# Kernel tuning notes

Measured on AMD Instinct MI355X. Metric: run time of the kernel, lower is better.

Reference implementation:

```python
import jax, jax.numpy as jnp
import numpy as np

B, N, IN, H, L, C = 2048, 100, 64, 256, 3, 3
NEG_SLOPE = 0.2


def setup_inputs() -> dict:
    key = jax.random.key(0)
    ks = jax.random.split(key, 11)
    s = lambda k, sh: jax.random.normal(k, sh, dtype=jnp.float32) * 0.05
    return {
        'x': jax.random.normal(ks[0], (B, N, IN), dtype=jnp.float32),
        'W_exp': s(ks[1], (IN, H)), 'b_exp': s(ks[2], (H,)),
        'W_l': s(ks[3], (L, H, H)), 'b_l': s(ks[4], (L, H)),
        'W_r': s(ks[5], (L, H, H)), 'b_r': s(ks[6], (L, H)),
        'att': s(ks[7], (L, H)), 'bias': s(ks[8], (L, H)),
        'W_fc': s(ks[9], (H, C)), 'b_fc': s(ks[10], (C,)),
    }


def _make_pe(n, d):
    pos = jnp.arange(n, dtype=jnp.float32)[:, None]
    div = jnp.exp(jnp.arange(0, d, 2, dtype=jnp.float32) * (-jnp.log(jnp.float32(10000.0)) / d))
    pe = jnp.zeros((n, d), dtype=jnp.float32)
    pe = pe.at[:, 0::2].set(jnp.sin(pos * div))
    pe = pe.at[:, 1::2].set(jnp.cos(pos * div))
    return pe


def _edges(n):
    # bidirectional chain + self loops (GATv2Conv add_self_loops=True)
    src = np.concatenate([np.arange(n - 1), np.arange(1, n), np.arange(n)])
    dst = np.concatenate([np.arange(1, n), np.arange(n - 1), np.arange(n)])
    return jnp.asarray(src), jnp.asarray(dst)


def _gatv2_conv(x, src, dst, Wl, bl, Wr, br, a, b, n):
    # x: [B,N,H]; PyG GATv2Conv, heads=1, share_weights=False
    xl = x @ Wl + bl                      # source transform [B,N,H]
    xr = x @ Wr + br                      # target transform [B,N,H]
    m = jax.nn.leaky_relu(xl[:, src] + xr[:, dst], NEG_SLOPE)   # [B,E,H]
    logits = jnp.einsum('beh,h->be', m, a)                      # [B,E]
    seg_max = jax.vmap(lambda l: jax.ops.segment_max(l, dst, num_segments=n))(logits)
    ex = jnp.exp(logits - seg_max[:, dst])
    denom = jax.vmap(lambda e: jax.ops.segment_sum(e, dst, num_segments=n))(ex)
    alpha = ex / denom[:, dst]                                  # [B,E]
    msgs = alpha[:, :, None] * xl[:, src]                       # [B,E,H]
    out = jax.vmap(lambda mm: jax.ops.segment_sum(mm, dst, num_segments=n))(msgs)
    return out + b


def reference(x, W_exp, b_exp, W_l, b_l, W_r, b_r, att, bias, W_fc, b_fc):
    n = x.shape[1]
    src, dst = _edges(n)
    x0 = x @ W_exp + b_exp + _make_pe(n, W_exp.shape[1])   # expander + positional encoding
    # Faithful to original: the loop feeds batch.x (= x0) into every conv layer,
    # so the output of the loop is the LAST conv applied to x0.
    h = x0
    for l in range(W_l.shape[0]):
        h = _gatv2_conv(x0, src, dst, W_l[l], b_l[l], W_r[l], b_r[l], att[l], bias[l], n)
    pooled = h.sum(axis=1)                                 # global_add_pool -> [B,H]
    return pooled @ W_fc + b_fc                            # [B,num_classes]
```

## Files before the change

### kernel.cpp

```cpp
#include <hip/hip_runtime.h>
#include <hip/hip_bf16.h>
#include <hip/hip_fp16.h>

#define BB 2048
#define NN 100
#define INF_ 64
#define HH 256
#define CC 3
#define QP 72

typedef __attribute__((ext_vector_type(8))) _Float16 h8v;
typedef __attribute__((ext_vector_type(2))) _Float16 h2v;
typedef __attribute__((ext_vector_type(2))) __fp16   g2v;
typedef __attribute__((ext_vector_type(4))) float f4v;

static __device__ __forceinline__ unsigned int pkh(float lo, float hi) {
    union { g2v g; unsigned int u; } c;
    c.g = __builtin_amdgcn_cvt_pkrtz(lo, hi);
    return c.u;
}

__global__ __launch_bounds__(256) void precompute_k(
    const float* __restrict__ W_exp, const float* __restrict__ b_exp,
    const float* __restrict__ W_l, const float* __restrict__ b_l,
    const float* __restrict__ W_r, const float* __restrict__ b_r,
    float* __restrict__ Wcomb, float* __restrict__ cadd)
{
    int r = blockIdx.x;
    int z = blockIdx.y;
    int t = threadIdx.x;
    const float* Wg = (z ? W_r : W_l) + 2 * HH * HH;
    const float* bg = (z ? b_r : b_l) + 2 * HH;

    __shared__ float sa[HH];
    float a;
    if (r < INF_) {
        a = W_exp[r * HH + t];
    } else {
        int n = r - INF_;
        float div = expf((float)(t & 254) * (-0.03597789207803f));
        float ang = (float)n * div;
        a = b_exp[t] + ((t & 1) ? cosf(ang) : sinf(ang));
    }
    sa[t] = a;
    __syncthreads();

    float acc = 0.f;
    #pragma unroll 8
    for (int h = 0; h < HH; ++h)
        acc += sa[h] * Wg[h * HH + t];

    if (r < INF_) Wcomb[(z * INF_ + r) * HH + t] = acc;
    else          cadd[(z * NN + (r - INF_)) * HH + t] = acc + bg[t];
}

#define N_WF 32768
#define N_CF4 14336

__global__ __launch_bounds__(256) void rearrange_k(
    const float* __restrict__ Wcomb, const float* __restrict__ cadd,
    unsigned short* __restrict__ WF, float* __restrict__ CFf)
{
    int i = blockIdx.x * 256 + threadIdx.x;
    if (i < N_WF) {
        int j = i & 7, lane = (i >> 3) & 63, ks = (i >> 9) & 1;
        int nt = (i >> 10) & 15, z = (i >> 14) & 1;
        int k = ks * 32 + 4 * (lane >> 4) + (j & 3) + 16 * (j >> 2);
        int n = nt * 16 + (lane & 15);
        __half h = __float2half(Wcomb[(z * INF_ + k) * HH + n]);
        WF[i] = __half_as_ushort(h);
    } else if (i < N_WF + N_CF4) {
        int i2 = i - N_WF;
        int lane = i2 & 63, nt = (i2 >> 6) & 15;
        int zm = i2 >> 10;
        int mt = zm % 7, z = zm / 7;
        int node = mt * 16 + (lane & 15);
        int feat = nt * 16 + (lane >> 4) * 4;
        float4 v = {0.f, 0.f, 0.f, 0.f};
        if (node < NN)
            v = *(const float4*)&cadd[(z * NN + node) * HH + feat];
        *(float4*)&CFf[(size_t)i2 * 4] = v;
    }
}

__global__ __launch_bounds__(512, 6) void fused_k(
    const float* __restrict__ x,
    const unsigned short* __restrict__ WF, const float* __restrict__ CFf,
    const float* __restrict__ Wcomb, const float* __restrict__ cadd,
    const float* __restrict__ att, const float* __restrict__ bias,
    const float* __restrict__ Wfc, const float* __restrict__ bfc,
    float* __restrict__ out)
{
    __shared__ unsigned short sxl[NN * QP];
    __shared__ unsigned short sxr[NN * QP];
    __shared__ unsigned short sxs[896 * 8];
    __shared__ unsigned int satt2[HH / 2];

    int b = blockIdx.x, t = threadIdx.x;
    int wave = t >> 6, lane = t & 63, g = lane >> 4, li = lane & 15;

    if (t < HH / 2) satt2[t] = pkh(att[2 * HH + 2 * t], att[2 * HH + 2 * t + 1]);

    const float* xb = x + (size_t)b * (NN * INF_);
    for (int s = t; s < 896; s += 512) {
        int sl = s & 63, ks = (s >> 6) & 1, mt = s >> 7;
        int m = mt * 16 + (sl & 15), gg = sl >> 4;
        union { h8v v; unsigned int u[4]; } a;
        if (m < NN) {
            float4 u = *(const float4*)&xb[m * INF_ + ks * 32 + 4 * gg];
            float4 v = *(const float4*)&xb[m * INF_ + ks * 32 + 16 + 4 * gg];
            a.u[0] = pkh(u.x, u.y);
            a.u[1] = pkh(u.z, u.w);
            a.u[2] = pkh(v.x, v.y);
            a.u[3] = pkh(v.z, v.w);
        } else {
            a.u[0] = a.u[1] = a.u[2] = a.u[3] = 0u;
        }
        *(h8v*)&sxs[s * 8] = a.v;
    }

    int q8 = t >> 3, c8 = (t & 7) * 8;
    int eBL[5], eBR[5];
    bool eva[5];
    float pv[5], pa[5];
    #pragma unroll
    for (int i = 0; i < 5; ++i) {
        int e = q8 + 64 * i;
        bool inr = (e < 300);
        int es = inr ? (e / 3) : 0;
        int ed = es + (e - 3 * es) - 1;
        bool v = inr && ed >= 0 && ed < NN;
        eva[i] = v;
        int dd = v ? ed : 0;
        eBL[i] = 2 * (es * QP + c8);
        eBR[i] = 2 * (dd * QP + c8);
        pv[i] = 0.f; pa[i] = 0.f;
    }

    int z = wave >> 2;
    int ntw = wave & 3;
    __syncthreads();

    #pragma unroll
    for (int q = 0; q < 4; ++q) {
        int nt = q * 4 + ntw;
        const h8v* bp = (const h8v*)WF + (size_t)(z * 16 + nt) * 2 * 64;
        h8v w0 = bp[lane];
        h8v w1 = bp[64 + lane];
        const h8v* sp = (const h8v*)sxs;
        unsigned short* dstp = z ? sxr : sxl;
        int colbase = ntw * 16 + g * 4;
        #pragma unroll
        for (int mt = 0; mt < 7; ++mt) {
            f4v c = *(const f4v*)&CFf[((size_t)((z * 7 + mt) * 16 + nt) * 64 + lane) * 4];
            h8v a0 = sp[mt * 128 + lane];
            h8v a1 = sp[mt * 128 + 64 + lane];
            c = __builtin_amdgcn_mfma_f32_16x16x32_f16(w0, a0, c, 0, 0, 0);
            c = __builtin_amdgcn_mfma_f32_16x16x32_f16(w1, a1, c, 0, 0, 0);
            int node = mt * 16 + li;
            if (mt < 6 || li < 4) {
                unsigned int lo = pkh(c[0], c[1]);
                unsigned int hi = pkh(c[2], c[3]);
                int elem = node * QP + colbase;
                uint2 wv2 = { lo, hi };
                *(uint2*)&dstp[elem] = wv2;
            }
        }
        __syncthreads();

        uint4 atv = *(const uint4*)&satt2[q * 32 + (t & 7) * 4];
        #pragma unroll
        for (int i = 0; i < 5; ++i) {
            if (eva[i]) {
                uint4 ua = *(const uint4*)((const char*)sxl + eBL[i]);
                uint4 ub = *(const uint4*)((const char*)sxr + eBR[i]);
                float fv = 0.f, fa = 0.f;
                #define PROC(UA, UB, AT) { \
                    union UU { unsigned int u; h2v h; g2v g; }; \
                    UU xa, xb2, vv, va, at; \
                    xa.u = (UA); xb2.u = (UB); at.u = (AT); \
                    vv.h = xa.h + xb2.h;               \
                    va.u = vv.u & 0x7FFF7FFFu;         \
                    fv = __builtin_amdgcn_fdot2(at.g, vv.g, fv, false); \
                    fa = __builtin_amdgcn_fdot2(at.g, va.g, fa, false); }
                PROC(ua.x, ub.x, atv.x);
                PROC(ua.y, ub.y, atv.y);
                PROC(ua.z, ub.z, atv.z);
                PROC(ua.w, ub.w, atv.w);
                #undef PROC
                pv[i] += fv; pa[i] += fa;
            }
        }
        __syncthreads();
    }

    float* lg      = (float*)sxs;
    float* wvp     = lg + 304;
    float* partial = wvp + 104;
    float* ypart   = partial + 16;

    #pragma unroll
    for (int i = 0; i < 5; ++i) {
        float s = fmaf(0.6f, pv[i], 0.4f * pa[i]);
        s += __shfl_xor(s, 1, 64);
        s += __shfl_xor(s, 2, 64);
        s += __shfl_xor(s, 4, 64);
        int e = q8 + 64 * i;
        if ((t & 7) == 0 && e < 300)
            lg[e] = eva[i] ? s : -1e30f;
    }
    __syncthreads();

    if (t < NN) {
        int i = t;
        float w = 0.f;
        #pragma unroll
        for (int dj = -1; dj <= 1; ++dj) {
            int j = i + dj;
            if (j < 0 || j >= NN) continue;
            float l0 = (j - 1 >= 0) ? lg[3 * (j - 1) + 2] : -1e30f;
            float l1 = lg[3 * j + 1];
            float l2 = (j + 1 < NN) ? lg[3 * (j + 1) + 0] : -1e30f;
            float mx = fmaxf(fmaxf(l0, l1), l2);
            float den = expf(l0 - mx) + expf(l1 - mx) + expf(l2 - mx);
            float myl = lg[3 * i + dj + 1];
            w += expf(myl - mx) / den;
        }
        wvp[i] = w;
    }
    __syncthreads();

    {
        int r0 = wave * 13;
        int r1 = (r0 + 13 < NN) ? r0 + 13 : NN;
        float acc = 0.f;
        for (int i = r0; i < r1; ++i)
            acc = fmaf(wvp[i], xb[i * INF_ + lane], acc);
        ypart[wave * 64 + lane] = acc;
    }
    __syncthreads();
    if (t < 64) {
        float s = 0.f;
        #pragma unroll
        for (int w = 0; w < 8; ++w) s += ypart[w * 64 + t];
        ypart[t] = s;
    }
    __syncthreads();

    if (t < HH) {
        float p = 100.f * bias[2 * HH + t];
        #pragma unroll
        for (int k = 0; k < INF_; k += 4) {
            float4 y4 = *(const float4*)&ypart[k];
            p = fmaf(y4.x, Wcomb[(k + 0) * HH + t], p);
            p = fmaf(y4.y, Wcomb[(k + 1) * HH + t], p);
            p = fmaf(y4.z, Wcomb[(k + 2) * HH + t], p);
            p = fmaf(y4.w, Wcomb[(k + 3) * HH + t], p);
        }
        #pragma unroll
        for (int i = 0; i < NN; i += 4) {
            float4 w4 = *(const float4*)&wvp[i];
            p = fmaf(w4.x, cadd[(i + 0) * HH + t], p);
            p = fmaf(w4.y, cadd[(i + 1) * HH + t], p);
            p = fmaf(w4.z, cadd[(i + 2) * HH + t], p);
            p = fmaf(w4.w, cadd[(i + 3) * HH + t], p);
        }

        float p0 = p * Wfc[t * 3 + 0];
        float p1 = p * Wfc[t * 3 + 1];
        float p2 = p * Wfc[t * 3 + 2];
        #pragma unroll
        for (int off = 32; off; off >>= 1) {
            p0 += __shfl_down(p0, off, 64);
            p1 += __shfl_down(p1, off, 64);
            p2 += __shfl_down(p2, off, 64);
        }
        if (lane == 0) {
            partial[wave * 3 + 0] = p0;
            partial[wave * 3 + 1] = p1;
            partial[wave * 3 + 2] = p2;
        }
    }
    __syncthreads();
    if (t < CC) {
        out[(size_t)b * CC + t] =
            partial[0 * 3 + t] + partial[1 * 3 + t] +
            partial[2 * 3 + t] + partial[3 * 3 + t] + bfc[t];
    }
}

extern "C" void kernel_launch(void* const* d_in, const int* in_sizes, int n_in,
                              void* d_out, int out_size, void* d_ws, size_t ws_size,
                              hipStream_t stream) {
    const float* x     = (const float*)d_in[0];
    const float* W_exp = (const float*)d_in[1];
    const float* b_exp = (const float*)d_in[2];
    const float* W_l   = (const float*)d_in[3];
    const float* b_l   = (const float*)d_in[4];
    const float* W_r   = (const float*)d_in[5];
    const float* b_r   = (const float*)d_in[6];
    const float* att   = (const float*)d_in[7];
    const float* bias  = (const float*)d_in[8];
    const float* W_fc  = (const float*)d_in[9];
    const float* b_fc  = (const float*)d_in[10];
    float* out = (float*)d_out;

    char* ws = (char*)d_ws;
    float* Wcomb = (float*)ws;
    float* cadd  = (float*)(ws + 131072);
    unsigned short* WF = (unsigned short*)(ws + 131072 + 204800);
    float* CFf = (float*)(ws + 131072 + 204800 + 65536);

    precompute_k<<<dim3(164, 2), 256, 0, stream>>>(W_exp, b_exp, W_l, b_l, W_r, b_r,
                                                   Wcomb, cadd);
    rearrange_k<<<184, 256, 0, stream>>>(Wcomb, cadd, WF, CFf);
    fused_k<<<BB, 512, 0, stream>>>(x, WF, CFf, Wcomb, cadd, att, bias, W_fc, b_fc, out);
}
```

Measured before the change: 81.41 us.

## Give each wave private feature slices to remove per-quarter block barriers

After: 94.10 us. +15.6%, slower.

```diff
diff --git a/kernel.cpp b/kernel.cpp
--- a/kernel.cpp
+++ b/kernel.cpp
@@ -7,7 +7,6 @@
 #define INF_ 64
 #define HH 256
 #define CC 3
-#define QP 72
 
 typedef __attribute__((ext_vector_type(8))) _Float16 h8v;
 typedef __attribute__((ext_vector_type(2))) _Float16 h2v;
@@ -83,7 +82,7 @@
     }
 }
 
-__global__ __launch_bounds__(512, 6) void fused_k(
+__global__ __launch_bounds__(512, 4) void fused_k(
     const float* __restrict__ x,
     const unsigned short* __restrict__ WF, const float* __restrict__ CFf,
     const float* __restrict__ Wcomb, const float* __restrict__ cadd,
@@ -91,8 +90,7 @@
     const float* __restrict__ Wfc, const float* __restrict__ bfc,
     float* __restrict__ out)
 {
-    __shared__ unsigned short sxl[NN * QP];
-    __shared__ unsigned short sxr[NN * QP];
+    __shared__ unsigned short sxw[8 * 2 * NN * 16];
     __shared__ unsigned short sxs[896 * 8];
     __shared__ unsigned int satt2[HH / 2];
 
@@ -119,61 +117,64 @@
         *(h8v*)&sxs[s * 8] = a.v;
     }
 
-    int q8 = t >> 3, c8 = (t & 7) * 8;
-    int eBL[5], eBR[5];
+    int baseL = (wave * 2 + 0) * (NN * 16);
+    int baseR = (wave * 2 + 1) * (NN * 16);
+    int eL[5], eR[5];
     bool eva[5];
     float pv[5], pa[5];
     #pragma unroll
     for (int i = 0; i < 5; ++i) {
-        int e = q8 + 64 * i;
+        int e = lane + 64 * i;
         bool inr = (e < 300);
         int es = inr ? (e / 3) : 0;
         int ed = es + (e - 3 * es) - 1;
         bool v = inr && ed >= 0 && ed < NN;
         eva[i] = v;
-        int dd = v ? ed : 0;
-        eBL[i] = 2 * (es * QP + c8);
-        eBR[i] = 2 * (dd * QP + c8);
+        eL[i] = baseL + es * 16;
+        eR[i] = baseR + (v ? ed : 0) * 16;
         pv[i] = 0.f; pa[i] = 0.f;
     }
-
-    int z = wave >> 2;
-    int ntw = wave & 3;
-    __syncthreads();
+    __syncthreads();
+
+    const h8v* WFp = (const h8v*)WF;
+    const f4v* CF4 = (const f4v*)CFf;
+    const h8v* sp  = (const h8v*)sxs;
 
     #pragma unroll
-    for (int q = 0; q < 4; ++q) {
-        int nt = q * 4 + ntw;
-        const h8v* bp = (const h8v*)WF + (size_t)(z * 16 + nt) * 2 * 64;
-        h8v w0 = bp[lane];
-        h8v w1 = bp[64 + lane];
-        const h8v* sp = (const h8v*)sxs;
-        unsigned short* dstp = z ? sxr : sxl;
-        int colbase = ntw * 16 + g * 4;
+    for (int h = 0; h < 2; ++h) {
+        int ntq = h * 8 + wave;
+        h8v w0l = WFp[((0 * 16 + ntq) * 2 + 0) * 64 + lane];
+        h8v w1l = WFp[((0 * 16 + ntq) * 2 + 1) * 64 + lane];
+        h8v w0r = WFp[((1 * 16 + ntq) * 2 + 0) * 64 + lane];
+        h8v w1r = WFp[((1 * 16 + ntq) * 2 + 1) * 64 + lane];
         #pragma unroll
         for (int mt = 0; mt < 7; ++mt) {
-            f4v c = *(const f4v*)&CFf[((size_t)((z * 7 + mt) * 16 + nt) * 64 + lane) * 4];
             h8v a0 = sp[mt * 128 + lane];
             h8v a1 = sp[mt * 128 + 64 + lane];
-            c = __builtin_amdgcn_mfma_f32_16x16x32_f16(w0, a0, c, 0, 0, 0);
-            c = __builtin_amdgcn_mfma_f32_16x16x32_f16(w1, a1, c, 0, 0, 0);
+            f4v c0 = CF4[((0 * 7 + mt) * 16 + ntq) * 64 + lane];
+            c0 = __builtin_amdgcn_mfma_f32_16x16x32_f16(w0l, a0, c0, 0, 0, 0);
+            c0 = __builtin_amdgcn_mfma_f32_16x16x32_f16(w1l, a1, c0, 0, 0, 0);
+            f4v c1 = CF4[((1 * 7 + mt) * 16 + ntq) * 64 + lane];
+            c1 = __builtin_amdgcn_mfma_f32_16x16x32_f16(w0r, a0, c1, 0, 0, 0);
+            c1 = __builtin_amdgcn_mfma_f32_16x16x32_f16(w1r, a1, c1, 0, 0, 0);
             int node = mt * 16 + li;
             if (mt < 6 || li < 4) {
-                unsigned int lo = pkh(c[0], c[1]);
-                unsigned int hi = pkh(c[2], c[3]);
-                int elem = node * QP + colbase;
-                uint2 wv2 = { lo, hi };
-                *(uint2*)&dstp[elem] = wv2;
+                int el = node * 16 + g * 4;
+                uint2 v0 = { pkh(c0[0], c0[1]), pkh(c0[2], c0[3]) };
+                uint2 v1 = { pkh(c1[0], c1[1]), pkh(c1[2], c1[3]) };
+                *(uint2*)&sxw[baseL + el] = v0;
+                *(uint2*)&sxw[baseR + el] = v1;
             }
         }
-        __syncthreads();
-
-        uint4 atv = *(const uint4*)&satt2[q * 32 + (t & 7) * 4];
+        uint4 atv0 = *(const uint4*)&satt2[h * 64 + wave * 8];
+        uint4 atv1 = *(const uint4*)&satt2[h * 64 + wave * 8 + 4];
         #pragma unroll
         for (int i = 0; i < 5; ++i) {
             if (eva[i]) {
-                uint4 ua = *(const uint4*)((const char*)sxl + eBL[i]);
-                uint4 ub = *(const uint4*)((const char*)sxr + eBR[i]);
+                uint4 ua0 = *(const uint4*)&sxw[eL[i]];
+                uint4 ua1 = *(const uint4*)&sxw[eL[i] + 8];
+                uint4 ub0 = *(const uint4*)&sxw[eR[i]];
+                uint4 ub1 = *(const uint4*)&sxw[eR[i] + 8];
                 float fv = 0.f, fa = 0.f;
                 #define PROC(UA, UB, AT) { \
                     union UU { unsigned int u; h2v h; g2v g; }; \
@@ -183,31 +184,39 @@
                     va.u = vv.u & 0x7FFF7FFFu;         \
                     fv = __builtin_amdgcn_fdot2(at.g, vv.g, fv, false); \
                     fa = __builtin_amdgcn_fdot2(at.g, va.g, fa, false); }
-                PROC(ua.x, ub.x, atv.x);
-                PROC(ua.y, ub.y, atv.y);
-                PROC(ua.z, ub.z, atv.z);
-                PROC(ua.w, ub.w, atv.w);
+                PROC(ua0.x, ub0.x, atv0.x);
+                PROC(ua0.y, ub0.y, atv0.y);
+                PROC(ua0.z, ub0.z, atv0.z);
+                PROC(ua0.w, ub0.w, atv0.w);
+                PROC(ua1.x, ub1.x, atv1.x);
+                PROC(ua1.y, ub1.y, atv1.y);
+                PROC(ua1.z, ub1.z, atv1.z);
+                PROC(ua1.w, ub1.w, atv1.w);
                 #undef PROC
                 pv[i] += fv; pa[i] += fa;
             }
         }
-        __syncthreads();
-    }
-
-    float* lg      = (float*)sxs;
+    }
+
+    __syncthreads();
+    float* spart = (float*)sxs;
+    #pragma unroll
+    for (int i = 0; i < 5; ++i) {
+        float s = eva[i] ? fmaf(0.6f, pv[i], 0.4f * pa[i]) : -1e30f;
+        spart[wave * 320 + lane + 64 * i] = s;
+    }
+    __syncthreads();
+
+    float* lg      = (float*)sxw;
     float* wvp     = lg + 304;
     float* partial = wvp + 104;
     float* ypart   = partial + 16;
 
-    #pragma unroll
-    for (int i = 0; i < 5; ++i) {
-        float s = fmaf(0.6f, pv[i], 0.4f * pa[i]);
-        s += __shfl_xor(s, 1, 64);
-        s += __shfl_xor(s, 2, 64);
-        s += __shfl_xor(s, 4, 64);
-        int e = q8 + 64 * i;
-        if ((t & 7) == 0 && e < 300)
-            lg[e] = eva[i] ? s : -1e30f;
+    if (t < 300) {
+        float s = 0.f;
+        #pragma unroll
+        for (int w = 0; w < 8; ++w) s += spart[w * 320 + t];
+        lg[t] = s;
     }
     __syncthreads();
 
@@ -275,7 +284,7 @@
             p1 += __shfl_down(p1, off, 64);
             p2 += __shfl_down(p2, off, 64);
         }
-        if (lane == 0) {
+        if ((t & 63) == 0) {
             partial[wave * 3 + 0] = p0;
             partial[wave * 3 + 1] = p1;
             partial[wave * 3 + 2] = p2;
```

## Compute per-edge pre-activations directly via MFMA on concatenated src/dst inputs

Applied to the files above, without the earlier changes.

Result: slower. 98.46 us (+20.9%).

```diff
diff --git a/kernel.cpp b/kernel.cpp
--- a/kernel.cpp
+++ b/kernel.cpp
@@ -7,10 +7,9 @@
 #define INF_ 64
 #define HH 256
 #define CC 3
-#define QP 72
+#define NET 19
 
 typedef __attribute__((ext_vector_type(8))) _Float16 h8v;
-typedef __attribute__((ext_vector_type(2))) _Float16 h2v;
 typedef __attribute__((ext_vector_type(2))) __fp16   g2v;
 typedef __attribute__((ext_vector_type(4))) float f4v;
 
@@ -55,11 +54,11 @@
 }
 
 #define N_WF 32768
-#define N_CF4 14336
+#define N_CFE4 19456
 
 __global__ __launch_bounds__(256) void rearrange_k(
     const float* __restrict__ Wcomb, const float* __restrict__ cadd,
-    unsigned short* __restrict__ WF, float* __restrict__ CFf)
+    unsigned short* __restrict__ WF, float* __restrict__ CFE)
 {
     int i = blockIdx.x * 256 + threadIdx.x;
     if (i < N_WF) {
@@ -69,37 +68,35 @@
         int n = nt * 16 + (lane & 15);
         __half h = __float2half(Wcomb[(z * INF_ + k) * HH + n]);
         WF[i] = __half_as_ushort(h);
-    } else if (i < N_WF + N_CF4) {
+    } else if (i < N_WF + N_CFE4) {
         int i2 = i - N_WF;
-        int lane = i2 & 63, nt = (i2 >> 6) & 15;
-        int zm = i2 >> 10;
-        int mt = zm % 7, z = zm / 7;
-        int node = mt * 16 + (lane & 15);
+        int lane = i2 & 63, nt = (i2 >> 6) & 15, et = i2 >> 10;
+        int edge = et * 16 + (lane & 15);
+        if (edge > 299) edge = 299;
+        int src = edge / 3;
+        int dst = src + (edge - 3 * src) - 1;
+        dst = dst < 0 ? 0 : (dst > NN - 1 ? NN - 1 : dst);
         int feat = nt * 16 + (lane >> 4) * 4;
-        float4 v = {0.f, 0.f, 0.f, 0.f};
-        if (node < NN)
-            v = *(const float4*)&cadd[(z * NN + node) * HH + feat];
-        *(float4*)&CFf[(size_t)i2 * 4] = v;
-    }
-}
-
-__global__ __launch_bounds__(512, 6) void fused_k(
+        float4 a = *(const float4*)&cadd[(0 * NN + src) * HH + feat];
+        float4 b = *(const float4*)&cadd[(1 * NN + dst) * HH + feat];
+        float4 v = { a.x + b.x, a.y + b.y, a.z + b.z, a.w + b.w };
+        *(float4*)&CFE[(size_t)i2 * 4] = v;
+    }
+}
+
+__global__ __launch_bounds__(512, 4) void fused_k(
     const float* __restrict__ x,
-    const unsigned short* __restrict__ WF, const float* __restrict__ CFf,
+    const unsigned short* __restrict__ WF, const float* __restrict__ CFE,
     const float* __restrict__ Wcomb, const float* __restrict__ cadd,
     const float* __restrict__ att, const float* __restrict__ bias,
     const float* __restrict__ Wfc, const float* __restrict__ bfc,
     float* __restrict__ out)
 {
-    __shared__ unsigned short sxl[NN * QP];
-    __shared__ unsigned short sxr[NN * QP];
     __shared__ unsigned short sxs[896 * 8];
-    __shared__ unsigned int satt2[HH / 2];
+    __shared__ float spart[8][304];
 
     int b = blockIdx.x, t = threadIdx.x;
     int wave = t >> 6, lane = t & 63, g = lane >> 4, li = lane & 15;
-
-    if (t < HH / 2) satt2[t] = pkh(att[2 * HH + 2 * t], att[2 * HH + 2 * t + 1]);
 
     const float* xb = x + (size_t)b * (NN * INF_);
     for (int s = t; s < 896; s += 512) {
@@ -119,95 +116,75 @@
         *(h8v*)&sxs[s * 8] = a.v;
     }
 
-    int q8 = t >> 3, c8 = (t & 7) * 8;
-    int eBL[5], eBR[5];
-    bool eva[5];
-    float pv[5], pa[5];
-    #pragma unroll
-    for (int i = 0; i < 5; ++i) {
-        int e = q8 + 64 * i;
-        bool inr = (e < 300);
-        int es = inr ? (e / 3) : 0;
-        int ed = es + (e - 3 * es) - 1;
-        bool v = inr && ed >= 0 && ed < NN;
-        eva[i] = v;
-        int dd = v ? ed : 0;
-        eBL[i] = 2 * (es * QP + c8);
-        eBR[i] = 2 * (dd * QP + c8);
-        pv[i] = 0.f; pa[i] = 0.f;
-    }
-
-    int z = wave >> 2;
-    int ntw = wave & 3;
-    __syncthreads();
-
-    #pragma unroll
-    for (int q = 0; q < 4; ++q) {
-        int nt = q * 4 + ntw;
-        const h8v* bp = (const h8v*)WF + (size_t)(z * 16 + nt) * 2 * 64;
-        h8v w0 = bp[lane];
-        h8v w1 = bp[64 + lane];
-        const h8v* sp = (const h8v*)sxs;
-        unsigned short* dstp = z ? sxr : sxl;
-        int colbase = ntw * 16 + g * 4;
-        #pragma unroll
-        for (int mt = 0; mt < 7; ++mt) {
-            f4v c = *(const f4v*)&CFf[((size_t)((z * 7 + mt) * 16 + nt) * 64 + lane) * 4];
-            h8v a0 = sp[mt * 128 + lane];
-            h8v a1 = sp[mt * 128 + 64 + lane];
-            c = __builtin_amdgcn_mfma_f32_16x16x32_f16(w0, a0, c, 0, 0, 0);
-            c = __builtin_amdgcn_mfma_f32_16x16x32_f16(w1, a1, c, 0, 0, 0);
-            int node = mt * 16 + li;
-            if (mt < 6 || li < 4) {
-                unsigned int lo = pkh(c[0], c[1]);
-                unsigned int hi = pkh(c[2], c[3]);
-                int elem = node * QP + colbase;
-                uint2 wv2 = { lo, hi };
-                *(uint2*)&dstp[elem] = wv2;
-            }
-        }
-        __syncthreads();
-
-        uint4 atv = *(const uint4*)&satt2[q * 32 + (t & 7) * 4];
-        #pragma unroll
-        for (int i = 0; i < 5; ++i) {
-            if (eva[i]) {
-                uint4 ua = *(const uint4*)((const char*)sxl + eBL[i]);
-                uint4 ub = *(const uint4*)((const char*)sxr + eBR[i]);
-                float fv = 0.f, fa = 0.f;
-                #define PROC(UA, UB, AT) { \
-                    union UU { unsigned int u; h2v h; g2v g; }; \
-                    UU xa, xb2, vv, va, at; \
-                    xa.u = (UA); xb2.u = (UB); at.u = (AT); \
-                    vv.h = xa.h + xb2.h;               \
-                    va.u = vv.u & 0x7FFF7FFFu;         \
-                    fv = __builtin_amdgcn_fdot2(at.g, vv.g, fv, false); \
-                    fa = __builtin_amdgcn_fdot2(at.g, va.g, fa, false); }
-                PROC(ua.x, ub.x, atv.x);
-                PROC(ua.y, ub.y, atv.y);
-                PROC(ua.z, ub.z, atv.z);
-                PROC(ua.w, ub.w, atv.w);
-                #undef PROC
-                pv[i] += fv; pa[i] += fa;
-            }
-        }
-        __syncthreads();
-    }
+    int nt0 = wave * 2;
+    const h8v* WFp = (const h8v*)WF;
+    h8v wA0 = WFp[((0 * 16 + nt0) * 2 + 0) * 64 + lane];
+    h8v wA1 = WFp[((0 * 16 + nt0) * 2 + 1) * 64 + lane];
+    h8v wA2 = WFp[((1 * 16 + nt0) * 2 + 0) * 64 + lane];
+    h8v wA3 = WFp[((1 * 16 + nt0) * 2 + 1) * 64 + lane];
+    h8v wB0 = WFp[((0 * 16 + nt0 + 1) * 2 + 0) * 64 + lane];
+    h8v wB1 = WFp[((0 * 16 + nt0 + 1) * 2 + 1) * 64 + lane];
+    h8v wB2 = WFp[((1 * 16 + nt0 + 1) * 2 + 0) * 64 + lane];
+    h8v wB3 = WFp[((1 * 16 + nt0 + 1) * 2 + 1) * 64 + lane];
+    f4v aA = *(const f4v*)&att[2 * HH + nt0 * 16 + g * 4];
+    f4v aB = *(const f4v*)&att[2 * HH + (nt0 + 1) * 16 + g * 4];
+
+    __syncthreads();
+
+    const h8v* sp = (const h8v*)sxs;
+    const f4v* CFE4 = (const f4v*)CFE;
+
+    for (int et = 0; et < NET; ++et) {
+        int edge = et * 16 + li;
+        bool eok = (edge < 300);
+        int ec = eok ? edge : 299;
+        int src = ec / 3;
+        int dst = src + (ec - 3 * src) - 1;
+        int dstc = dst < 0 ? 0 : (dst > NN - 1 ? NN - 1 : dst);
+        int slotS = (src >> 4) * 128 + g * 16 + (src & 15);
+        int slotD = (dstc >> 4) * 128 + g * 16 + (dstc & 15);
+        h8v e0 = sp[slotS];
+        h8v e1 = sp[slotS + 64];
+        h8v e2 = sp[slotD];
+        h8v e3 = sp[slotD + 64];
+
+        f4v c0 = CFE4[(et * 16 + nt0) * 64 + lane];
+        f4v c1 = CFE4[(et * 16 + nt0 + 1) * 64 + lane];
+        c0 = __builtin_amdgcn_mfma_f32_16x16x32_f16(wA0, e0, c0, 0, 0, 0);
+        c1 = __builtin_amdgcn_mfma_f32_16x16x32_f16(wB0, e0, c1, 0, 0, 0);
+        c0 = __builtin_amdgcn_mfma_f32_16x16x32_f16(wA1, e1, c0, 0, 0, 0);
+        c1 = __builtin_amdgcn_mfma_f32_16x16x32_f16(wB1, e1, c1, 0, 0, 0);
+        c0 = __builtin_amdgcn_mfma_f32_16x16x32_f16(wA2, e2, c0, 0, 0, 0);
+        c1 = __builtin_amdgcn_mfma_f32_16x16x32_f16(wB2, e2, c1, 0, 0, 0);
+        c0 = __builtin_amdgcn_mfma_f32_16x16x32_f16(wA3, e3, c0, 0, 0, 0);
+        c1 = __builtin_amdgcn_mfma_f32_16x16x32_f16(wB3, e3, c1, 0, 0, 0);
+
+        float sv = 0.f, sa = 0.f;
+        #pragma unroll
+        for (int r = 0; r < 4; ++r) {
+            float v0 = c0[r];
+            sv = fmaf(aA[r], v0, sv); sa = fmaf(aA[r], fabsf(v0), sa);
+            float v1 = c1[r];
+            sv = fmaf(aB[r], v1, sv); sa = fmaf(aB[r], fabsf(v1), sa);
+        }
+        float s = fmaf(0.6f, sv, 0.4f * sa);
+        s += __shfl_xor(s, 16, 64);
+        s += __shfl_xor(s, 32, 64);
+        if (lane < 16 && eok)
+            spart[wave][et * 16 + lane] = s;
+    }
+    __syncthreads();
 
     float* lg      = (float*)sxs;
     float* wvp     = lg + 304;
-    float* partial = wvp + 104;
+    float* partial = wvp + 108;
     float* ypart   = partial + 16;
 
-    #pragma unroll
-    for (int i = 0; i < 5; ++i) {
-        float s = fmaf(0.6f, pv[i], 0.4f * pa[i]);
-        s += __shfl_xor(s, 1, 64);
-        s += __shfl_xor(s, 2, 64);
-        s += __shfl_xor(s, 4, 64);
-        int e = q8 + 64 * i;
-        if ((t & 7) == 0 && e < 300)
-            lg[e] = eva[i] ? s : -1e30f;
+    if (t < 300) {
+        float s = 0.f;
+        #pragma unroll
+        for (int w = 0; w < 8; ++w) s += spart[w][t];
+        lg[t] = s;
     }
     __syncthreads();
 
@@ -259,11 +236,11 @@
         }
         #pragma unroll
         for (int i = 0; i < NN; i += 4) {
-            float4 w4 = *(const float4*)&wvp[i];
-            p = fmaf(w4.x, cadd[(i + 0) * HH + t], p);
-            p = fmaf(w4.y, cadd[(i + 1) * HH + t], p);
-            p = fmaf(w4.z, cadd[(i + 2) * HH + t], p);
-            p = fmaf(w4.w, cadd[(i + 3) * HH + t], p);
+            float4 w4v = *(const float4*)&wvp[i];
+            p = fmaf(w4v.x, cadd[(i + 0) * HH + t], p);
+            p = fmaf(w4v.y, cadd[(i + 1) * HH + t], p);
+            p = fmaf(w4v.z, cadd[(i + 2) * HH + t], p);
+            p = fmaf(w4v.w, cadd[(i + 3) * HH + t], p);
         }
 
         float p0 = p * Wfc[t * 3 + 0];
@@ -309,10 +286,10 @@
     float* Wcomb = (float*)ws;
     float* cadd  = (float*)(ws + 131072);
     unsigned short* WF = (unsigned short*)(ws + 131072 + 204800);
-    float* CFf = (float*)(ws + 131072 + 204800 + 65536);
+    float* CFE = (float*)(ws + 131072 + 204800 + 65536);
 
     precompute_k<<<dim3(164, 2), 256, 0, stream>>>(W_exp, b_exp, W_l, b_l, W_r, b_r,
                                                    Wcomb, cadd);
-    rearrange_k<<<184, 256, 0, stream>>>(Wcomb, cadd, WF, CFf);
-    fused_k<<<BB, 512, 0, stream>>>(x, WF, CFf, Wcomb, cadd, att, bias, W_fc, b_fc, out);
-}
+    rearrange_k<<<204, 256, 0, stream>>>(Wcomb, cadd, WF, CFE);
+    fused_k<<<BB, 512, 0, stream>>>(x, WF, CFE, Wcomb, cadd, att, bias, W_fc, b_fc, out);
+}
```
